# Kernel optimization log

Measured on AMD Instinct MI355X. Metric: run time of the kernel, lower is better.

## Reference

```python
import jax, jax.numpy as jnp
import numpy as np

TOP_K = 8

def setup_inputs() -> dict:
    key = jax.random.key(0)
    k1, k2 = jax.random.split(key)
    hidden_states = jax.random.normal(k1, (4, 4096, 4096), dtype=jnp.float32)
    W_router = jax.random.normal(k2, (64, 4096), dtype=jnp.float32) * (1.0 / np.sqrt(4096))
    return {"hidden_states": hidden_states, "W_router": W_router}

def reference(hidden_states, W_router):
    # router_logits = hidden @ W^T : [B, S, E]
    router_logits = jnp.einsum('bsh,eh->bse', hidden_states, W_router)
    B, S, E = router_logits.shape
    logits_2d = router_logits.reshape(-1, E)  # [B*S, E]
    probs = jax.nn.softmax(logits_2d, axis=-1)  # numerically stable softmax
    topk_probs, topk_idx = jax.lax.top_k(probs, TOP_K)
    routing_weights = topk_probs / jnp.sum(topk_probs, axis=-1, keepdims=True)
    return (routing_weights.reshape(B, S, TOP_K), topk_idx.reshape(B, S, TOP_K))
```

## Files before the change

### kernel.cpp

```cpp
#include <hip/hip_runtime.h>
#include <math.h>

typedef __attribute__((ext_vector_type(4))) float f32x4;
typedef __attribute__((ext_vector_type(8))) short short8;
typedef __attribute__((ext_vector_type(4))) unsigned int u32x4;

#define KDIM  4096
#define NTOK  16384
#define BT    64
#define KHALF 1024
#define CH    (KHALF/32)
#define DELTA 1.2e-4f

union S8U { u32x4 u; short8 s; };
__device__ inline short8 as_s8(u32x4 v) { S8U t; t.u = v; return t.s; }

__device__ inline void splitpair(float x0, float x1, unsigned& hp, unsigned& lp) {
  unsigned u0 = __float_as_uint(x0) + 0x8000u;
  unsigned u1 = __float_as_uint(x1) + 0x8000u;
  hp = (u0 >> 16) | (u1 & 0xffff0000u);
  float h0 = __uint_as_float(u0 & 0xffff0000u);
  float h1 = __uint_as_float(u1 & 0xffff0000u);
  float l0 = x0 - h0;
  float l1 = x1 - h1;
  unsigned v0 = __float_as_uint(l0) + 0x8000u;
  unsigned v1 = __float_as_uint(l1) + 0x8000u;
  lp = (v0 >> 16) | (v1 & 0xffff0000u);
}

#define LOADA(st, c) do { \
  apf[st][0] = *(const f32x4*)(Arow + (size_t)(c) * 32); \
  apf[st][1] = *(const f32x4*)(Arow + (size_t)(c) * 32 + 4); \
  apf[st][2] = *(const f32x4*)(Arow + 16 * KDIM + (size_t)(c) * 32); \
  apf[st][3] = *(const f32x4*)(Arow + 16 * KDIM + (size_t)(c) * 32 + 4); \
} while (0)

#define LOADW(st, c) do { \
  _Pragma("unroll") \
  for (int nf_ = 0; nf_ < 4; ++nf_) { \
    wpf[st][nf_ * 2]     = *(const f32x4*)(Wrow + (size_t)nf_ * 16 * KDIM + (size_t)(c) * 32); \
    wpf[st][nf_ * 2 + 1] = *(const f32x4*)(Wrow + (size_t)nf_ * 16 * KDIM + (size_t)(c) * 32 + 4); \
  } \
} while (0)

#define STEP(J) do { \
  const int c_ = cc + (J); \
  u32x4 ahv[2], alv[2], bhv[4], blv[4]; \
  _Pragma("unroll") for (int rt = 0; rt < 2; ++rt) \
    _Pragma("unroll") for (int q = 0; q < 4; ++q) { \
      float x0 = apf[(J) & 3][rt * 2 + (q >> 1)][(q & 1) * 2]; \
      float x1 = apf[(J) & 3][rt * 2 + (q >> 1)][(q & 1) * 2 + 1]; \
      unsigned hp, lp; splitpair(x0, x1, hp, lp); \
      ahv[rt][q] = hp; alv[rt][q] = lp; } \
  _Pragma("unroll") for (int nf = 0; nf < 4; ++nf) \
    _Pragma("unroll") for (int q = 0; q < 4; ++q) { \
      float x0 = wpf[(J) & 1][nf * 2 + (q >> 1)][(q & 1) * 2]; \
      float x1 = wpf[(J) & 1][nf * 2 + (q >> 1)][(q & 1) * 2 + 1]; \
      unsigned hp, lp; splitpair(x0, x1, hp, lp); \
      bhv[nf][q] = hp; blv[nf][q] = lp; } \
  if (c_ + 4 < CH) LOADA((J) & 3, c_ + 4); \
  if (c_ + 2 < CH) LOADW((J) & 1, c_ + 2); \
  _Pragma("unroll") for (int rt = 0; rt < 2; ++rt) \
    _Pragma("unroll") for (int nf = 0; nf < 4; ++nf) { \
      acc[rt][nf] = __builtin_amdgcn_mfma_f32_16x16x32_bf16(as_s8(ahv[rt]), as_s8(bhv[nf]), acc[rt][nf], 0, 0, 0); \
      acc[rt][nf] = __builtin_amdgcn_mfma_f32_16x16x32_bf16(as_s8(ahv[rt]), as_s8(blv[nf]), acc[rt][nf], 0, 0, 0); \
      acc[rt][nf] = __builtin_amdgcn_mfma_f32_16x16x32_bf16(as_s8(alv[rt]), as_s8(bhv[nf]), acc[rt][nf], 0, 0, 0); \
    } \
} while (0)

__global__ __launch_bounds__(512, 2) void router_kernel(
    const float* __restrict__ H, const float* __restrict__ W,
    float* __restrict__ out)
{
  __shared__ float  LG[BT][68];
  __shared__ double dlog[64];
  __shared__ int    refList[BT];
  __shared__ int    refCnt;

  const int tid  = threadIdx.x;
  const int lane = tid & 63;
  const int wv   = tid >> 6;
  const int tg   = wv >> 2;
  const int kh   = wv & 3;
  const int l15  = lane & 15;
  const int kg8  = (lane >> 4) * 8;
  const int tb   = blockIdx.x * BT;

  if (tid == 0) refCnt = 0;

  const float* Arow = H + (size_t)(tb + tg * 32 + l15) * KDIM + (size_t)kh * KHALF + kg8;
  const float* Wrow = W + (size_t)l15 * KDIM + (size_t)kh * KHALF + kg8;

  f32x4 acc[2][4] = {};
  f32x4 apf[4][4];
  f32x4 wpf[2][8];

  LOADA(0, 0); LOADA(1, 1); LOADA(2, 2); LOADA(3, 3);
  LOADW(0, 0); LOADW(1, 1);

  #pragma unroll 1
  for (int cc = 0; cc < CH; cc += 4) {
    STEP(0); STEP(1); STEP(2); STEP(3);
  }

  #pragma unroll 1
  for (int kk = 0; kk < 4; ++kk) {
    if (kh == kk) {
      #pragma unroll
      for (int rt = 0; rt < 2; ++rt)
        #pragma unroll
        for (int nf = 0; nf < 4; ++nf)
          #pragma unroll
          for (int r = 0; r < 4; ++r) {
            int tt  = tg * 32 + rt * 16 + (lane >> 4) * 4 + r;
            int col = nf * 16 + l15;
            if (kk == 0) LG[tt][col]  = acc[rt][nf][r];
            else         LG[tt][col] += acc[rt][nf][r];
          }
    }
    __syncthreads();
  }

  for (int t8 = 0; t8 < 8; ++t8) {
    int t = wv * 8 + t8;
    float x = LG[t][lane];
    float m = x;
    #pragma unroll
    for (int off = 32; off > 0; off >>= 1)
      m = fmaxf(m, __shfl_xor(m, off, 64));
    float v = x;
    float selV = 0.f, sum = 0.f, prev = 0.f, gapmin = 1e30f;
    int   selI = 0;
    #pragma unroll
    for (int j = 0; j < 9; ++j) {
      float bv = v;
      int   bi = lane;
      #pragma unroll
      for (int off = 32; off > 0; off >>= 1) {
        float ov = __shfl_xor(bv, off, 64);
        int   oi = __shfl_xor(bi, off, 64);
        if (ov > bv || (ov == bv && oi < bi)) { bv = ov; bi = oi; }
      }
      if (j > 0) gapmin = fminf(gapmin, prev - bv);
      prev = bv;
      if (j < 8) {
        float e = __expf(bv - m);
        sum += e;
        if (lane == j) { selV = e; selI = bi; }
      }
      if (lane == bi) v = -INFINITY;
    }
    bool flag = (gapmin < DELTA);
    if (flag && lane == 0) {
      int p = atomicAdd(&refCnt, 1);
      refList[p] = t;
    }
    if (!flag && lane < 8) {
      int tgl = tb + t;
      out[(size_t)tgl * 8 + lane] = selV / sum;
      out[(size_t)NTOK * 8 + (size_t)tgl * 8 + lane] = (float)selI;
    }
  }
  __syncthreads();

  const int nref = refCnt;
  const int re = tid >> 3;
  const int rs = tid & 7;
  for (int i = 0; i < nref; ++i) {
    const int t = refList[i];
    const float* hrow = H + (size_t)(tb + t) * KDIM;
    const float* wrw  = W + (size_t)re * KDIM;
    double accd = 0.0;
    for (int k0 = 0; k0 < KDIM; k0 += 32) {
      f32x4 hv = *reinterpret_cast<const f32x4*>(hrow + k0 + rs * 4);
      f32x4 wvv = *reinterpret_cast<const f32x4*>(wrw + k0 + rs * 4);
      #pragma unroll
      for (int j = 0; j < 4; ++j)
        accd = fma((double)hv[j], (double)wvv[j], accd);
    }
    accd += __shfl_xor(accd, 1, 64);
    accd += __shfl_xor(accd, 2, 64);
    accd += __shfl_xor(accd, 4, 64);
    if (rs == 0) dlog[re] = accd;
    __syncthreads();
    if (tid < 64) {
      double x = dlog[tid];
      double m = x;
      #pragma unroll
      for (int off = 32; off > 0; off >>= 1)
        m = fmax(m, __shfl_xor(m, off, 64));
      double v = x, sum = 0.0, selV = 0.0;
      int selI = 0;
      #pragma unroll
      for (int j = 0; j < 8; ++j) {
        double bv = v;
        int    bi = tid;
        #pragma unroll
        for (int off = 32; off > 0; off >>= 1) {
          double ov = __shfl_xor(bv, off, 64);
          int    oi = __shfl_xor(bi, off, 64);
          if (ov > bv || (ov == bv && oi < bi)) { bv = ov; bi = oi; }
        }
        double e = exp(bv - m);
        sum += e;
        if (tid == j) { selV = e; selI = bi; }
        if (tid == bi) v = -1e300;
      }
      if (tid < 8) {
        int tgl = tb + t;
        out[(size_t)tgl * 8 + tid] = (float)(selV / sum);
        out[(size_t)NTOK * 8 + (size_t)tgl * 8 + tid] = (float)selI;
      }
    }
    __syncthreads();
  }
}

extern "C" void kernel_launch(void* const* d_in, const int* in_sizes, int n_in,
                              void* d_out, int out_size, void* d_ws, size_t ws_size,
                              hipStream_t stream) {
  const float* H = (const float*)d_in[0];
  const float* W = (const float*)d_in[1];
  float* out = (float*)d_out;
  router_kernel<<<NTOK / BT, 512, 0, stream>>>(H, W, out);
}
```

Baseline: 201.2 us.

## Pre-split router weights into bf16 hi/lo once and shrink token tile

Adds a small pre-pass kernel that splits W into bf16 high/low pairs in the workspace, so the main kernel loads pre-split weights instead of re-splitting them in every block. The token tile drops from 64 to 16 per block, using 256 threads with four waves each covering a quarter of K, which gives 1024 blocks instead of 256. The per-wave K partials are reduced through shared memory in one pass instead of four serialized accumulate passes. Each block now reads W per 16 tokens, so total W traffic rises, mostly from L2, and a second kernel launch is added.

```diff
diff --git a/kernel.cpp b/kernel.cpp
--- a/kernel.cpp
+++ b/kernel.cpp
@@ -7,72 +7,84 @@
 
 #define KDIM  4096
 #define NTOK  16384
-#define BT    64
-#define KHALF 1024
-#define CH    (KHALF/32)
+#define BT    16
+#define KSL   1024
+#define CH    (KSL/32)
 #define DELTA 1.2e-4f
 
 union S8U { u32x4 u; short8 s; };
 __device__ inline short8 as_s8(u32x4 v) { S8U t; t.u = v; return t.s; }
 
-__device__ inline void splitpair(float x0, float x1, unsigned& hp, unsigned& lp) {
+struct HiLo { unsigned h, l; };
+
+__device__ inline HiLo splitpair(float x0, float x1) {
   unsigned u0 = __float_as_uint(x0) + 0x8000u;
   unsigned u1 = __float_as_uint(x1) + 0x8000u;
-  hp = (u0 >> 16) | (u1 & 0xffff0000u);
+  HiLo r;
+  r.h = (u0 >> 16) | (u1 & 0xffff0000u);
   float h0 = __uint_as_float(u0 & 0xffff0000u);
   float h1 = __uint_as_float(u1 & 0xffff0000u);
   float l0 = x0 - h0;
   float l1 = x1 - h1;
   unsigned v0 = __float_as_uint(l0) + 0x8000u;
   unsigned v1 = __float_as_uint(l1) + 0x8000u;
-  lp = (v0 >> 16) | (v1 & 0xffff0000u);
+  r.l = (v0 >> 16) | (v1 & 0xffff0000u);
+  return r;
+}
+
+__global__ __launch_bounds__(512) void wsplit_kernel(
+    const float* __restrict__ W, char* __restrict__ ws)
+{
+  int gid = blockIdx.x * 512 + threadIdx.x;
+  const float* p = W + (size_t)gid * 8;
+  f32x4 x0 = ((const f32x4*)p)[0];
+  f32x4 x1 = ((const f32x4*)p)[1];
+  u32x4 hi, lo;
+  HiLo s;
+  s = splitpair(x0[0], x0[1]); hi[0] = s.h; lo[0] = s.l;
+  s = splitpair(x0[2], x0[3]); hi[1] = s.h; lo[1] = s.l;
+  s = splitpair(x1[0], x1[1]); hi[2] = s.h; lo[2] = s.l;
+  s = splitpair(x1[2], x1[3]); hi[3] = s.h; lo[3] = s.l;
+  *(u32x4*)(ws + (size_t)gid * 32)      = hi;
+  *(u32x4*)(ws + (size_t)gid * 32 + 16) = lo;
 }
 
 #define LOADA(st, c) do { \
   apf[st][0] = *(const f32x4*)(Arow + (size_t)(c) * 32); \
   apf[st][1] = *(const f32x4*)(Arow + (size_t)(c) * 32 + 4); \
-  apf[st][2] = *(const f32x4*)(Arow + 16 * KDIM + (size_t)(c) * 32); \
-  apf[st][3] = *(const f32x4*)(Arow + 16 * KDIM + (size_t)(c) * 32 + 4); \
 } while (0)
 
 #define LOADW(st, c) do { \
   _Pragma("unroll") \
   for (int nf_ = 0; nf_ < 4; ++nf_) { \
-    wpf[st][nf_ * 2]     = *(const f32x4*)(Wrow + (size_t)nf_ * 16 * KDIM + (size_t)(c) * 32); \
-    wpf[st][nf_ * 2 + 1] = *(const f32x4*)(Wrow + (size_t)nf_ * 16 * KDIM + (size_t)(c) * 32 + 4); \
+    wph[st][nf_] = *(const u32x4*)(Wbase + (size_t)nf_ * 262144 + (size_t)(c) * 128); \
+    wpl[st][nf_] = *(const u32x4*)(Wbase + (size_t)nf_ * 262144 + (size_t)(c) * 128 + 16); \
   } \
 } while (0)
 
 #define STEP(J) do { \
   const int c_ = cc + (J); \
-  u32x4 ahv[2], alv[2], bhv[4], blv[4]; \
-  _Pragma("unroll") for (int rt = 0; rt < 2; ++rt) \
-    _Pragma("unroll") for (int q = 0; q < 4; ++q) { \
-      float x0 = apf[(J) & 3][rt * 2 + (q >> 1)][(q & 1) * 2]; \
-      float x1 = apf[(J) & 3][rt * 2 + (q >> 1)][(q & 1) * 2 + 1]; \
-      unsigned hp, lp; splitpair(x0, x1, hp, lp); \
-      ahv[rt][q] = hp; alv[rt][q] = lp; } \
-  _Pragma("unroll") for (int nf = 0; nf < 4; ++nf) \
-    _Pragma("unroll") for (int q = 0; q < 4; ++q) { \
-      float x0 = wpf[(J) & 1][nf * 2 + (q >> 1)][(q & 1) * 2]; \
-      float x1 = wpf[(J) & 1][nf * 2 + (q >> 1)][(q & 1) * 2 + 1]; \
-      unsigned hp, lp; splitpair(x0, x1, hp, lp); \
-      bhv[nf][q] = hp; blv[nf][q] = lp; } \
+  u32x4 ah, al; \
+  HiLo s0 = splitpair(apf[(J) & 3][0][0], apf[(J) & 3][0][1]); \
+  HiLo s1 = splitpair(apf[(J) & 3][0][2], apf[(J) & 3][0][3]); \
+  HiLo s2 = splitpair(apf[(J) & 3][1][0], apf[(J) & 3][1][1]); \
+  HiLo s3 = splitpair(apf[(J) & 3][1][2], apf[(J) & 3][1][3]); \
+  ah[0] = s0.h; al[0] = s0.l; ah[1] = s1.h; al[1] = s1.l; \
+  ah[2] = s2.h; al[2] = s2.l; ah[3] = s3.h; al[3] = s3.l; \
   if (c_ + 4 < CH) LOADA((J) & 3, c_ + 4); \
+  _Pragma("unroll") for (int nf = 0; nf < 4; ++nf) { \
+    acc[nf] = __builtin_amdgcn_mfma_f32_16x16x32_bf16(as_s8(ah), as_s8(wph[(J) & 1][nf]), acc[nf], 0, 0, 0); \
+    acc[nf] = __builtin_amdgcn_mfma_f32_16x16x32_bf16(as_s8(ah), as_s8(wpl[(J) & 1][nf]), acc[nf], 0, 0, 0); \
+    acc[nf] = __builtin_amdgcn_mfma_f32_16x16x32_bf16(as_s8(al), as_s8(wph[(J) & 1][nf]), acc[nf], 0, 0, 0); \
+  } \
   if (c_ + 2 < CH) LOADW((J) & 1, c_ + 2); \
-  _Pragma("unroll") for (int rt = 0; rt < 2; ++rt) \
-    _Pragma("unroll") for (int nf = 0; nf < 4; ++nf) { \
-      acc[rt][nf] = __builtin_amdgcn_mfma_f32_16x16x32_bf16(as_s8(ahv[rt]), as_s8(bhv[nf]), acc[rt][nf], 0, 0, 0); \
-      acc[rt][nf] = __builtin_amdgcn_mfma_f32_16x16x32_bf16(as_s8(ahv[rt]), as_s8(blv[nf]), acc[rt][nf], 0, 0, 0); \
-      acc[rt][nf] = __builtin_amdgcn_mfma_f32_16x16x32_bf16(as_s8(alv[rt]), as_s8(bhv[nf]), acc[rt][nf], 0, 0, 0); \
-    } \
 } while (0)
 
-__global__ __launch_bounds__(512, 2) void router_kernel(
-    const float* __restrict__ H, const float* __restrict__ W,
-    float* __restrict__ out)
+__global__ __launch_bounds__(256, 4) void router_kernel(
+    const float* __restrict__ H, const char* __restrict__ Ws,
+    const float* __restrict__ W, float* __restrict__ out)
 {
-  __shared__ float  LG[BT][68];
+  __shared__ float  LG[4][BT][68];
   __shared__ double dlog[64];
   __shared__ int    refList[BT];
   __shared__ int    refCnt;
@@ -80,20 +92,20 @@
   const int tid  = threadIdx.x;
   const int lane = tid & 63;
   const int wv   = tid >> 6;
-  const int tg   = wv >> 2;
-  const int kh   = wv & 3;
+  const int kh   = wv;
   const int l15  = lane & 15;
-  const int kg8  = (lane >> 4) * 8;
+  const int kg   = lane >> 4;
   const int tb   = blockIdx.x * BT;
 
   if (tid == 0) refCnt = 0;
 
-  const float* Arow = H + (size_t)(tb + tg * 32 + l15) * KDIM + (size_t)kh * KHALF + kg8;
-  const float* Wrow = W + (size_t)l15 * KDIM + (size_t)kh * KHALF + kg8;
-
-  f32x4 acc[2][4] = {};
-  f32x4 apf[4][4];
-  f32x4 wpf[2][8];
+  const float* Arow  = H  + (size_t)(tb + l15) * KDIM + (size_t)kh * KSL + kg * 8;
+  const char*  Wbase = Ws + (size_t)l15 * 16384 + (size_t)(kh * 128 + kg) * 32;
+
+  f32x4 acc[4] = {};
+  f32x4 apf[4][2];
+  u32x4 wph[2][4];
+  u32x4 wpl[2][4];
 
   LOADA(0, 0); LOADA(1, 1); LOADA(2, 2); LOADA(3, 3);
   LOADW(0, 0); LOADW(1, 1);
@@ -103,27 +115,16 @@
     STEP(0); STEP(1); STEP(2); STEP(3);
   }
 
-  #pragma unroll 1
-  for (int kk = 0; kk < 4; ++kk) {
-    if (kh == kk) {
-      #pragma unroll
-      for (int rt = 0; rt < 2; ++rt)
-        #pragma unroll
-        for (int nf = 0; nf < 4; ++nf)
-          #pragma unroll
-          for (int r = 0; r < 4; ++r) {
-            int tt  = tg * 32 + rt * 16 + (lane >> 4) * 4 + r;
-            int col = nf * 16 + l15;
-            if (kk == 0) LG[tt][col]  = acc[rt][nf][r];
-            else         LG[tt][col] += acc[rt][nf][r];
-          }
-    }
-    __syncthreads();
-  }
-
-  for (int t8 = 0; t8 < 8; ++t8) {
-    int t = wv * 8 + t8;
-    float x = LG[t][lane];
+  #pragma unroll
+  for (int nf = 0; nf < 4; ++nf)
+    #pragma unroll
+    for (int r = 0; r < 4; ++r)
+      LG[kh][kg * 4 + r][nf * 16 + l15] = acc[nf][r];
+  __syncthreads();
+
+  for (int t4 = 0; t4 < 4; ++t4) {
+    int t = wv * 4 + t4;
+    float x = ((LG[0][t][lane] + LG[1][t][lane]) + LG[2][t][lane]) + LG[3][t][lane];
     float m = x;
     #pragma unroll
     for (int off = 32; off > 0; off >>= 1)
@@ -164,14 +165,14 @@
   __syncthreads();
 
   const int nref = refCnt;
-  const int re = tid >> 3;
-  const int rs = tid & 7;
+  const int re = tid >> 2;
+  const int rs = tid & 3;
   for (int i = 0; i < nref; ++i) {
     const int t = refList[i];
     const float* hrow = H + (size_t)(tb + t) * KDIM;
     const float* wrw  = W + (size_t)re * KDIM;
     double accd = 0.0;
-    for (int k0 = 0; k0 < KDIM; k0 += 32) {
+    for (int k0 = 0; k0 < KDIM; k0 += 16) {
       f32x4 hv = *reinterpret_cast<const f32x4*>(hrow + k0 + rs * 4);
       f32x4 wvv = *reinterpret_cast<const f32x4*>(wrw + k0 + rs * 4);
       #pragma unroll
@@ -180,7 +181,6 @@
     }
     accd += __shfl_xor(accd, 1, 64);
     accd += __shfl_xor(accd, 2, 64);
-    accd += __shfl_xor(accd, 4, 64);
     if (rs == 0) dlog[re] = accd;
     __syncthreads();
     if (tid < 64) {
@@ -222,5 +222,7 @@
   const float* H = (const float*)d_in[0];
   const float* W = (const float*)d_in[1];
   float* out = (float*)d_out;
-  router_kernel<<<NTOK / BT, 512, 0, stream>>>(H, W, out);
-}
+  char*  ws  = (char*)d_ws;
+  wsplit_kernel<<<64, 512, 0, stream>>>(W, ws);
+  router_kernel<<<NTOK / BT, 256, 0, stream>>>(H, ws, W, out);
+}
```

Result: slower. 292.0 us (+45.2%).
